# Kernel tuning notes

Hardware: AMD Instinct MI355X
Metric: run time of the kernel (lower is better)

## Reference

```python
import jax, jax.numpy as jnp
import numpy as np

B, S, D, H = 4, 8192, 1024, 16
DK = D // H
EPS = 1e-6


def setup_inputs() -> dict:
    key = jax.random.key(0)
    ks = jax.random.split(key, 9)
    s = 1.0 / np.sqrt(D)
    return {
        "x": jax.random.normal(ks[0], (B, S, D), dtype=jnp.float32),
        "Wq": jax.random.normal(ks[1], (D, D), dtype=jnp.float32) * s,
        "bq": jax.random.normal(ks[2], (D,), dtype=jnp.float32) * s,
        "Wk": jax.random.normal(ks[3], (D, D), dtype=jnp.float32) * s,
        "bk": jax.random.normal(ks[4], (D,), dtype=jnp.float32) * s,
        "Wv": jax.random.normal(ks[5], (D, D), dtype=jnp.float32) * s,
        "bv": jax.random.normal(ks[6], (D,), dtype=jnp.float32) * s,
        "Wo": jax.random.normal(ks[7], (D, D), dtype=jnp.float32) * s,
        "bo": jax.random.normal(ks[8], (D,), dtype=jnp.float32) * s,
    }


def reference(x, Wq, bq, Wk, bk, Wv, bv, Wo, bo):
    # projections (torch Linear: x @ W.T + b), split heads -> [B, H, S, DK]
    def proj(W, b):
        return (x @ W.T + b).reshape(B, S, H, DK).transpose(0, 2, 1, 3)

    q = jax.nn.relu(proj(Wq, bq)) + EPS
    k = jax.nn.relu(proj(Wk, bk)) + EPS
    v = proj(Wv, bv)

    # kv state: [B, H, DK, DK]
    kv = jnp.einsum('bhsd,bhse->bhde', k, v)
    qkv = jnp.einsum('bhsd,bhde->bhse', q, kv)            # [B, H, S, DK]
    k_sum = k.sum(axis=2)                                  # [B, H, DK]
    q_k_sum = jnp.einsum('bhsd,bhd->bhs', q, k_sum)        # [B, H, S]
    out = qkv / (q_k_sum[..., None] + EPS)                 # [B, H, S, DK]

    out = out.transpose(0, 2, 1, 3).reshape(B, S, D)
    return out @ Wo.T + bo
```

## Files before the change

### kernel.cpp

```cpp
#include <hip/hip_runtime.h>
#include <hip/hip_bf16.h>

#define BB 4
#define SS 8192
#define DD 1024
#define HH 16
#define DKK 64
#define EPSV 1e-6f

typedef unsigned short u16;
typedef __attribute__((ext_vector_type(8))) short bf16x8v;
typedef __attribute__((ext_vector_type(4))) float f32x4v;

__device__ inline u16 f2bf(float f) {
    __hip_bfloat16 b = __float2bfloat16(f);
    return *reinterpret_cast<u16*>(&b);
}
__device__ inline float bf2f(u16 u) {
    union { unsigned int i; float f; } c; c.i = ((unsigned int)u) << 16; return c.f;
}

__device__ inline void gload_lds16(const void* g, void* l) {
    __builtin_amdgcn_global_load_lds(
        (const __attribute__((address_space(1))) void*)g,
        (__attribute__((address_space(3))) void*)l, 16, 0, 0);
}

__global__ __launch_bounds__(256)
void split_hilo(const float* __restrict__ in, u16* __restrict__ outp, int n4) {
    int i = blockIdx.x * 256 + threadIdx.x;
    if (i >= n4) return;
    size_t e = (size_t)i * 4;
    size_t row = e >> 10; int col = (int)(e & 1023);
    float4 v = *(const float4*)&in[e];
    ushort4 hi, lo;
    hi.x = f2bf(v.x); lo.x = f2bf(v.x - bf2f(hi.x));
    hi.y = f2bf(v.y); lo.y = f2bf(v.y - bf2f(hi.y));
    hi.z = f2bf(v.z); lo.z = f2bf(v.z - bf2f(hi.z));
    hi.w = f2bf(v.w); lo.w = f2bf(v.w - bf2f(hi.w));
    size_t ob = row * 2048 + col;
    *(ushort4*)&outp[ob] = hi;
    *(ushort4*)&outp[ob + 1024] = lo;
}

template<int EPI>
__global__ __launch_bounds__(512, 2)
void gemm_split(const u16* __restrict__ A, const u16* __restrict__ Wsp,
                const float* __restrict__ bias, void* __restrict__ out) {
    __shared__ u16 lds[65536];

    int bid = blockIdx.x;
    int tl  = (bid & 7) * 64 + (bid >> 3);
    const int m0 = (tl >> 2) * 256;
    const int n0 = (tl & 3) * 256;

    const int tid = threadIdx.x;
    const int w = tid >> 6, l = tid & 63;
    const int wr = (w >> 2) * 128;
    const int wc = (w & 3) * 64;
    const int aReg = (w >> 2) * 8192;
    const int bReg = 16384 + ((w & 3) >> 1) * 8192;
    const int bLoc = ((w & 3) & 1) * 64;

    f32x4v acc[8][4];
    #pragma unroll
    for (int i = 0; i < 8; ++i)
        #pragma unroll
        for (int j = 0; j < 4; ++j) acc[i][j] = (f32x4v)0.f;

    const int srow = l >> 3;
    const int scol = ((l & 7) ^ srow) << 3;

    const u16* Abase = A   + (size_t)m0 * 2048;
    const u16* Bbase = Wsp + (size_t)n0 * 2048;

    auto kaOf = [](int t) { int k0 = t * 64; return (k0 < 2048) ? k0 : k0 - 2048; };
    auto kwOf = [](int t) { int k0 = t * 64; return (k0 < 1024) ? k0 : k0 - 1024; };

    auto stageA = [&](int t, int half) {
        if (t >= 48) return;
        const u16* src = Abase + (size_t)(half * 128) * 2048 + kaOf(t) + scol;
        u16* dst = &lds[(t & 1) * 32768 + half * 8192];
        #pragma unroll
        for (int g = 0; g < 2; ++g) {
            int chunk = g * 8 + w;
            gload_lds16(src + (size_t)(chunk * 8 + srow) * 2048, dst + chunk * 512);
        }
    };
    auto stageB = [&](int t, int half) {
        if (t >= 48) return;
        const u16* src = Bbase + (size_t)(half * 128) * 2048 + kwOf(t) + scol;
        u16* dst = &lds[(t & 1) * 32768 + 16384 + half * 8192];
        #pragma unroll
        for (int g = 0; g < 2; ++g) {
            int chunk = g * 8 + w;
            gload_lds16(src + (size_t)(chunk * 8 + srow) * 2048, dst + chunk * 512);
        }
    };

    stageA(0, 0); stageA(0, 1); stageB(0, 0); stageB(0, 1);
    stageB(1, 0); stageB(1, 1);
    asm volatile("s_waitcnt vmcnt(4)" ::: "memory");
    __builtin_amdgcn_s_barrier();

    for (int t = 0; t < 48; ++t) {
        __builtin_amdgcn_sched_barrier(0);
        const char* aRg = (const char*)&lds[(t & 1) * 32768 + aReg];
        const char* bRg = (const char*)&lds[(t & 1) * 32768 + bReg];
        const int cb = (l >> 4) << 4;

        bf16x8v bF[4][2], aF[2][2];
        #pragma unroll
        for (int fn = 0; fn < 4; ++fn)
            #pragma unroll
            for (int ks = 0; ks < 2; ++ks) {
                int r = bLoc + fn * 16 + (l & 15);
                bF[fn][ks] = *(const bf16x8v*)(bRg + r * 128 + ((ks * 64 + cb) ^ ((r & 7) << 4)));
            }
        #pragma unroll
        for (int f = 0; f < 2; ++f)
            #pragma unroll
            for (int ks = 0; ks < 2; ++ks) {
                int r = f * 16 + (l & 15);
                aF[f][ks] = *(const bf16x8v*)(aRg + r * 128 + ((ks * 64 + cb) ^ ((r & 7) << 4)));
            }
        stageA(t + 1, 0);
        __builtin_amdgcn_s_barrier();
        asm volatile("s_waitcnt lgkmcnt(0)" ::: "memory");
        __builtin_amdgcn_s_setprio(1);
        #pragma unroll
        for (int f = 0; f < 2; ++f)
            #pragma unroll
            for (int fn = 0; fn < 4; ++fn)
                #pragma unroll
                for (int ks = 0; ks < 2; ++ks)
                    acc[f][fn] = __builtin_amdgcn_mfma_f32_16x16x32_bf16(
                        aF[f][ks], bF[fn][ks], acc[f][fn], 0, 0, 0);
        __builtin_amdgcn_s_setprio(0);
        __builtin_amdgcn_s_barrier();

        #pragma unroll
        for (int q = 1; q < 4; ++q) {
            #pragma unroll
            for (int f = 0; f < 2; ++f)
                #pragma unroll
                for (int ks = 0; ks < 2; ++ks) {
                    int r = q * 32 + f * 16 + (l & 15);
                    aF[f][ks] = *(const bf16x8v*)(aRg + r * 128 + ((ks * 64 + cb) ^ ((r & 7) << 4)));
                }
            if (q == 1)      stageA(t + 1, 1);
            else if (q == 2) stageB(t + 2, 0);
            else             stageB(t + 2, 1);
            __builtin_amdgcn_s_barrier();
            asm volatile("s_waitcnt lgkmcnt(0)" ::: "memory");
            __builtin_amdgcn_s_setprio(1);
            #pragma unroll
            for (int f = 0; f < 2; ++f)
                #pragma unroll
                for (int fn = 0; fn < 4; ++fn)
                    #pragma unroll
                    for (int ks = 0; ks < 2; ++ks)
                        acc[q * 2 + f][fn] = __builtin_amdgcn_mfma_f32_16x16x32_bf16(
                            aF[f][ks], bF[fn][ks], acc[q * 2 + f][fn], 0, 0, 0);
            __builtin_amdgcn_s_setprio(0);
            if (q == 3) asm volatile("s_waitcnt vmcnt(4)" ::: "memory");
            __builtin_amdgcn_s_barrier();
        }
    }

    float bv4[4];
    #pragma unroll
    for (int fn = 0; fn < 4; ++fn) bv4[fn] = bias[n0 + wc + fn * 16 + (l & 15)];

    #pragma unroll
    for (int mf = 0; mf < 8; ++mf)
        #pragma unroll
        for (int fn = 0; fn < 4; ++fn)
            #pragma unroll
            for (int r = 0; r < 4; ++r) {
                int m = m0 + wr + mf * 16 + ((l >> 4) << 2) + r;
                int n = n0 + wc + fn * 16 + (l & 15);
                float o = acc[mf][fn][r] + bv4[fn];
                if (EPI == 0 || EPI == 1) o = fmaxf(o, 0.f) + EPSV;
                if (EPI <= 2) {
                    int b = m >> 13, s = m & (SS - 1), h = n >> 6, d = n & 63;
                    size_t idx = (((size_t)b * HH + h) * SS + s) * DKK + d;
                    if (EPI == 0) ((float*)out)[idx] = o;
                    else          ((u16*)out)[idx]   = f2bf(o);
                } else {
                    ((float*)out)[(size_t)m * DD + n] = o;
                }
            }
}

__global__ __launch_bounds__(256)
void kv_ksum_kernel(const u16* __restrict__ k, const u16* __restrict__ v,
                    float* __restrict__ kv, float* __restrict__ ksum) {
    __shared__ float kt[64][64];
    __shared__ float vt[64][64];
    const int bh = blockIdx.y;
    const int tid = threadIdx.x;
    const int d0 = (tid >> 4) << 2;
    const int e0 = (tid & 15) << 2;
    float acc[4][4];
    #pragma unroll
    for (int i = 0; i < 4; ++i)
        #pragma unroll
        for (int j = 0; j < 4; ++j) acc[i][j] = 0.f;
    float ksl = 0.f;

    const size_t base = ((size_t)bh * SS + (size_t)blockIdx.x * 512) * DKK;
    for (int sub = 0; sub < 8; ++sub) {
        #pragma unroll
        for (int it = 0; it < 4; ++it) {
            int f = tid + it * 256;
            int r = f >> 4, c = (f & 15) << 2;
            ushort4 ku = *(const ushort4*)&k[base + sub * 4096 + (size_t)r * 64 + c];
            ushort4 vu = *(const ushort4*)&v[base + sub * 4096 + (size_t)r * 64 + c];
            *(float4*)&kt[r][c] = make_float4(bf2f(ku.x), bf2f(ku.y), bf2f(ku.z), bf2f(ku.w));
            *(float4*)&vt[r][c] = make_float4(bf2f(vu.x), bf2f(vu.y), bf2f(vu.z), bf2f(vu.w));
        }
        __syncthreads();
        for (int ss = 0; ss < 64; ++ss) {
            float4 ka = *(const float4*)&kt[ss][d0];
            float4 va = *(const float4*)&vt[ss][e0];
            float ar[4] = {ka.x, ka.y, ka.z, ka.w};
            float vr[4] = {va.x, va.y, va.z, va.w};
            #pragma unroll
            for (int i = 0; i < 4; ++i)
                #pragma unroll
                for (int j = 0; j < 4; ++j)
                    acc[i][j] = fmaf(ar[i], vr[j], acc[i][j]);
        }
        if (tid < 64) {
            for (int ss = 0; ss < 64; ++ss) ksl += kt[ss][tid];
        }
        __syncthreads();
    }
    float* kvb = kv + (size_t)bh * 4096;
    #pragma unroll
    for (int i = 0; i < 4; ++i)
        #pragma unroll
        for (int j = 0; j < 4; ++j)
            atomicAdd(&kvb[(d0 + i) * 64 + (e0 + j)], acc[i][j]);
    if (tid < 64) atomicAdd(&ksum[bh * 64 + tid], ksl);
}

__global__ __launch_bounds__(256)
void qkv_norm_kernel(const float* __restrict__ q, const float* __restrict__ kv,
                     const float* __restrict__ ksum, u16* __restrict__ mid) {
    __shared__ float kvs[64][65];
    __shared__ float ks[64];
    __shared__ float qrow[4][64];
    const int bh = blockIdx.y, b = bh >> 4, h = bh & 15;
    const int tid = threadIdx.x;
    for (int i = tid; i < 4096; i += 256) kvs[i >> 6][i & 63] = kv[(size_t)bh * 4096 + i];
    if (tid < 64) ks[tid] = ksum[bh * 64 + tid];
    __syncthreads();
    const int g = tid >> 6, lane = tid & 63;
    float kvc[64];
    #pragma unroll
    for (int d = 0; d < 64; ++d) kvc[d] = kvs[d][lane];
    const float ksl = ks[lane];
    const size_t qbase = (size_t)bh * SS * DKK;
    const int s0 = blockIdx.x * 256;
    for (int it = 0; it < 64; ++it) {
        int s = s0 + (it << 2) + g;
        float qv = q[qbase + (size_t)s * DKK + lane];
        qrow[g][lane] = qv;
        float qks = qv * ksl;
        #pragma unroll
        for (int off = 32; off >= 1; off >>= 1) qks += __shfl_xor(qks, off, 64);
        float o = 0.f;
        #pragma unroll
        for (int d4 = 0; d4 < 64; d4 += 4) {
            float4 qq = *(const float4*)&qrow[g][d4];
            o = fmaf(qq.x, kvc[d4 + 0], o);
            o = fmaf(qq.y, kvc[d4 + 1], o);
            o = fmaf(qq.z, kvc[d4 + 2], o);
            o = fmaf(qq.w, kvc[d4 + 3], o);
        }
        o = o / (qks + EPSV);
        u16 hi = f2bf(o);
        u16 lo = f2bf(o - bf2f(hi));
        size_t ob = ((size_t)b * SS + s) * 2048 + h * DKK + lane;
        mid[ob] = hi;
        mid[ob + 1024] = lo;
    }
}

extern "C" void kernel_launch(void* const* d_in, const int* in_sizes, int n_in,
                              void* d_out, int out_size, void* d_ws, size_t ws_size,
                              hipStream_t stream) {
    const float* x  = (const float*)d_in[0];
    const float* Wq = (const float*)d_in[1];
    const float* bq = (const float*)d_in[2];
    const float* Wk = (const float*)d_in[3];
    const float* bk = (const float*)d_in[4];
    const float* Wv = (const float*)d_in[5];
    const float* bv = (const float*)d_in[6];
    const float* Wo = (const float*)d_in[7];
    const float* bo = (const float*)d_in[8];

    char* ws = (char*)d_ws;
    u16*   xsplit  = (u16*)ws;
    u16*   wsplit  = (u16*)(ws + 134217728);
    u16*   k_ws    = (u16*)(ws + 138412032);
    u16*   v_ws    = (u16*)(ws + 205520896);
    float* kv_ws   = (float*)(ws + 272629760);
    float* ksum_ws = (float*)(ws + 273678336);
    u16*   midsplit = xsplit;
    float* q_ws    = (float*)d_out;

    split_hilo<<<32768, 256, 0, stream>>>(x, xsplit, 8388608);

    split_hilo<<<1024, 256, 0, stream>>>(Wq, wsplit, 262144);
    gemm_split<0><<<512, 512, 0, stream>>>(xsplit, wsplit, bq, (void*)q_ws);
    split_hilo<<<1024, 256, 0, stream>>>(Wk, wsplit, 262144);
    gemm_split<1><<<512, 512, 0, stream>>>(xsplit, wsplit, bk, (void*)k_ws);
    split_hilo<<<1024, 256, 0, stream>>>(Wv, wsplit, 262144);
    gemm_split<2><<<512, 512, 0, stream>>>(xsplit, wsplit, bv, (void*)v_ws);

    hipMemsetAsync(kv_ws, 0, 1048576 + 16384, stream);
    kv_ksum_kernel<<<dim3(16, 64), 256, 0, stream>>>(k_ws, v_ws, kv_ws, ksum_ws);
    qkv_norm_kernel<<<dim3(32, 64), 256, 0, stream>>>(q_ws, kv_ws, ksum_ws, midsplit);

    split_hilo<<<1024, 256, 0, stream>>>(Wo, wsplit, 262144);
    gemm_split<3><<<512, 512, 0, stream>>>(midsplit, wsplit, bo, d_out);
}
```

Before: 1.180 ms.

## Fuse K/V projections, fold q·ksum into Q GEMM epilogue, rework kv reduction

The K and V projections become one GEMM over a concatenated 2048-wide weight. The Q projection now runs after the kv/ksum pass, so its epilogue can compute the per-row q·ksum normaliser and the norm kernel no longer needs a shuffle reduction. The GEMM inner loop is reordered to load 4 A fragments against 2 B fragments per phase, and the kv reduction kernel now uses async LDS staging with 8x8 per-thread tiles and an in-block reduction before the atomics. This is meant to cut launches, redundant A-matrix reads and atomic traffic, at the cost of more register pressure and a new workspace layout.

```diff
diff --git a/kernel.cpp b/kernel.cpp
--- a/kernel.cpp
+++ b/kernel.cpp
@@ -43,16 +43,19 @@
     *(ushort4*)&outp[ob + 1024] = lo;
 }
 
-template<int EPI>
+template<int EPI, int NT>
 __global__ __launch_bounds__(512, 2)
 void gemm_split(const u16* __restrict__ A, const u16* __restrict__ Wsp,
-                const float* __restrict__ bias, void* __restrict__ out) {
+                const float* __restrict__ bias, const float* __restrict__ bias2,
+                void* __restrict__ out, void* __restrict__ out2,
+                const float* __restrict__ ksum, float* __restrict__ qks) {
     __shared__ u16 lds[65536];
 
+    constexpr int CHUNK = 128 * NT / 8;
     int bid = blockIdx.x;
-    int tl  = (bid & 7) * 64 + (bid >> 3);
-    const int m0 = (tl >> 2) * 256;
-    const int n0 = (tl & 3) * 256;
+    int tl  = (bid & 7) * CHUNK + (bid >> 3);
+    const int m0 = (tl / NT) * 256;
+    const int n0 = (tl % NT) * 256;
 
     const int tid = threadIdx.x;
     const int w = tid >> 6, l = tid & 63;
@@ -104,173 +107,278 @@
     __builtin_amdgcn_s_barrier();
 
     for (int t = 0; t < 48; ++t) {
-        __builtin_amdgcn_sched_barrier(0);
         const char* aRg = (const char*)&lds[(t & 1) * 32768 + aReg];
         const char* bRg = (const char*)&lds[(t & 1) * 32768 + bReg];
         const int cb = (l >> 4) << 4;
 
-        bf16x8v bF[4][2], aF[2][2];
-        #pragma unroll
-        for (int fn = 0; fn < 4; ++fn)
-            #pragma unroll
-            for (int ks = 0; ks < 2; ++ks) {
-                int r = bLoc + fn * 16 + (l & 15);
-                bF[fn][ks] = *(const bf16x8v*)(bRg + r * 128 + ((ks * 64 + cb) ^ ((r & 7) << 4)));
-            }
-        #pragma unroll
-        for (int f = 0; f < 2; ++f)
+        bf16x8v aF[4][2], bF0[2][2], bF1[2][2];
+        #pragma unroll
+        for (int f = 0; f < 4; ++f)
             #pragma unroll
             for (int ks = 0; ks < 2; ++ks) {
                 int r = f * 16 + (l & 15);
                 aF[f][ks] = *(const bf16x8v*)(aRg + r * 128 + ((ks * 64 + cb) ^ ((r & 7) << 4)));
             }
+        #pragma unroll
+        for (int f = 0; f < 2; ++f)
+            #pragma unroll
+            for (int ks = 0; ks < 2; ++ks) {
+                int r = bLoc + f * 16 + (l & 15);
+                bF0[f][ks] = *(const bf16x8v*)(bRg + r * 128 + ((ks * 64 + cb) ^ ((r & 7) << 4)));
+            }
         stageA(t + 1, 0);
         __builtin_amdgcn_s_barrier();
         asm volatile("s_waitcnt lgkmcnt(0)" ::: "memory");
         __builtin_amdgcn_s_setprio(1);
         #pragma unroll
-        for (int f = 0; f < 2; ++f)
-            #pragma unroll
-            for (int fn = 0; fn < 4; ++fn)
+        for (int f = 0; f < 4; ++f)
+            #pragma unroll
+            for (int fn = 0; fn < 2; ++fn)
                 #pragma unroll
                 for (int ks = 0; ks < 2; ++ks)
                     acc[f][fn] = __builtin_amdgcn_mfma_f32_16x16x32_bf16(
-                        aF[f][ks], bF[fn][ks], acc[f][fn], 0, 0, 0);
+                        aF[f][ks], bF0[fn][ks], acc[f][fn], 0, 0, 0);
         __builtin_amdgcn_s_setprio(0);
         __builtin_amdgcn_s_barrier();
 
         #pragma unroll
-        for (int q = 1; q < 4; ++q) {
-            #pragma unroll
-            for (int f = 0; f < 2; ++f)
-                #pragma unroll
-                for (int ks = 0; ks < 2; ++ks) {
-                    int r = q * 32 + f * 16 + (l & 15);
-                    aF[f][ks] = *(const bf16x8v*)(aRg + r * 128 + ((ks * 64 + cb) ^ ((r & 7) << 4)));
+        for (int f = 0; f < 2; ++f)
+            #pragma unroll
+            for (int ks = 0; ks < 2; ++ks) {
+                int r = bLoc + (2 + f) * 16 + (l & 15);
+                bF1[f][ks] = *(const bf16x8v*)(bRg + r * 128 + ((ks * 64 + cb) ^ ((r & 7) << 4)));
+            }
+        stageA(t + 1, 1);
+        __builtin_amdgcn_s_barrier();
+        asm volatile("s_waitcnt lgkmcnt(0)" ::: "memory");
+        __builtin_amdgcn_s_setprio(1);
+        #pragma unroll
+        for (int f = 0; f < 4; ++f)
+            #pragma unroll
+            for (int fn = 0; fn < 2; ++fn)
+                #pragma unroll
+                for (int ks = 0; ks < 2; ++ks)
+                    acc[f][2 + fn] = __builtin_amdgcn_mfma_f32_16x16x32_bf16(
+                        aF[f][ks], bF1[fn][ks], acc[f][2 + fn], 0, 0, 0);
+        __builtin_amdgcn_s_setprio(0);
+        __builtin_amdgcn_s_barrier();
+
+        #pragma unroll
+        for (int f = 0; f < 4; ++f)
+            #pragma unroll
+            for (int ks = 0; ks < 2; ++ks) {
+                int r = (4 + f) * 16 + (l & 15);
+                aF[f][ks] = *(const bf16x8v*)(aRg + r * 128 + ((ks * 64 + cb) ^ ((r & 7) << 4)));
+            }
+        stageB(t + 2, 0);
+        __builtin_amdgcn_s_barrier();
+        asm volatile("s_waitcnt lgkmcnt(0)" ::: "memory");
+        __builtin_amdgcn_s_setprio(1);
+        #pragma unroll
+        for (int f = 0; f < 4; ++f)
+            #pragma unroll
+            for (int fn = 0; fn < 2; ++fn)
+                #pragma unroll
+                for (int ks = 0; ks < 2; ++ks)
+                    acc[4 + f][fn] = __builtin_amdgcn_mfma_f32_16x16x32_bf16(
+                        aF[f][ks], bF0[fn][ks], acc[4 + f][fn], 0, 0, 0);
+        __builtin_amdgcn_s_setprio(0);
+        __builtin_amdgcn_s_barrier();
+
+        stageB(t + 2, 1);
+        __builtin_amdgcn_s_barrier();
+        __builtin_amdgcn_s_setprio(1);
+        #pragma unroll
+        for (int f = 0; f < 4; ++f)
+            #pragma unroll
+            for (int fn = 0; fn < 2; ++fn)
+                #pragma unroll
+                for (int ks = 0; ks < 2; ++ks)
+                    acc[4 + f][2 + fn] = __builtin_amdgcn_mfma_f32_16x16x32_bf16(
+                        aF[f][ks], bF1[fn][ks], acc[4 + f][2 + fn], 0, 0, 0);
+        __builtin_amdgcn_s_setprio(0);
+        asm volatile("s_waitcnt vmcnt(4)" ::: "memory");
+        __builtin_amdgcn_s_barrier();
+    }
+
+    const int lane15 = l & 15, lg = l >> 4;
+
+    if (EPI == 1) {
+        const bool isK = (n0 + wc) < 1024;
+        const int nb = (n0 + wc) - (isK ? 0 : 1024);
+        const float* bp = isK ? bias : bias2;
+        u16* outp = (u16*)(isK ? out : out2);
+        const int h = nb >> 6;
+        float bv4[4];
+        #pragma unroll
+        for (int fn = 0; fn < 4; ++fn) bv4[fn] = bp[nb + fn * 16 + lane15];
+        #pragma unroll
+        for (int mf = 0; mf < 8; ++mf)
+            #pragma unroll
+            for (int fn = 0; fn < 4; ++fn)
+                #pragma unroll
+                for (int r = 0; r < 4; ++r) {
+                    int m = m0 + wr + mf * 16 + lg * 4 + r;
+                    int b = m >> 13, s = m & (SS - 1);
+                    float o = acc[mf][fn][r] + bv4[fn];
+                    if (isK) o = fmaxf(o, 0.f) + EPSV;
+                    outp[(((size_t)b * HH + h) * SS + s) * DKK + fn * 16 + lane15] = f2bf(o);
                 }
-            if (q == 1)      stageA(t + 1, 1);
-            else if (q == 2) stageB(t + 2, 0);
-            else             stageB(t + 2, 1);
-            __builtin_amdgcn_s_barrier();
-            asm volatile("s_waitcnt lgkmcnt(0)" ::: "memory");
-            __builtin_amdgcn_s_setprio(1);
-            #pragma unroll
-            for (int f = 0; f < 2; ++f)
-                #pragma unroll
-                for (int fn = 0; fn < 4; ++fn)
-                    #pragma unroll
-                    for (int ks = 0; ks < 2; ++ks)
-                        acc[q * 2 + f][fn] = __builtin_amdgcn_mfma_f32_16x16x32_bf16(
-                            aF[f][ks], bF[fn][ks], acc[q * 2 + f][fn], 0, 0, 0);
-            __builtin_amdgcn_s_setprio(0);
-            if (q == 3) asm volatile("s_waitcnt vmcnt(4)" ::: "memory");
-            __builtin_amdgcn_s_barrier();
-        }
-    }
-
-    float bv4[4];
-    #pragma unroll
-    for (int fn = 0; fn < 4; ++fn) bv4[fn] = bias[n0 + wc + fn * 16 + (l & 15)];
-
-    #pragma unroll
-    for (int mf = 0; mf < 8; ++mf)
-        #pragma unroll
-        for (int fn = 0; fn < 4; ++fn)
+    } else if (EPI == 0) {
+        const int b = m0 >> 13, h = (n0 + wc) >> 6;
+        const int bh = b * HH + h;
+        float bv4[4], ksc[4];
+        #pragma unroll
+        for (int fn = 0; fn < 4; ++fn) {
+            bv4[fn] = bias[n0 + wc + fn * 16 + lane15];
+            ksc[fn] = ksum[(size_t)bh * 64 + fn * 16 + lane15];
+        }
+        float* qo = (float*)out;
+        #pragma unroll
+        for (int mf = 0; mf < 8; ++mf)
             #pragma unroll
             for (int r = 0; r < 4; ++r) {
-                int m = m0 + wr + mf * 16 + ((l >> 4) << 2) + r;
-                int n = n0 + wc + fn * 16 + (l & 15);
-                float o = acc[mf][fn][r] + bv4[fn];
-                if (EPI == 0 || EPI == 1) o = fmaxf(o, 0.f) + EPSV;
-                if (EPI <= 2) {
-                    int b = m >> 13, s = m & (SS - 1), h = n >> 6, d = n & 63;
-                    size_t idx = (((size_t)b * HH + h) * SS + s) * DKK + d;
-                    if (EPI == 0) ((float*)out)[idx] = o;
-                    else          ((u16*)out)[idx]   = f2bf(o);
-                } else {
-                    ((float*)out)[(size_t)m * DD + n] = o;
+                int m = m0 + wr + mf * 16 + lg * 4 + r;
+                int s = m & (SS - 1);
+                float part = 0.f;
+                #pragma unroll
+                for (int fn = 0; fn < 4; ++fn) {
+                    float o = fmaxf(acc[mf][fn][r] + bv4[fn], 0.f) + EPSV;
+                    qo[((size_t)bh * SS + s) * DKK + fn * 16 + lane15] = o;
+                    part += o * ksc[fn];
                 }
-            }
+                #pragma unroll
+                for (int msk = 1; msk < 16; msk <<= 1)
+                    part += __shfl_xor(part, msk, 16);
+                if (lane15 == 0) qks[(size_t)bh * SS + s] = part;
+            }
+    } else {
+        float bv4[4];
+        #pragma unroll
+        for (int fn = 0; fn < 4; ++fn) bv4[fn] = bias[n0 + wc + fn * 16 + lane15];
+        float* op = (float*)out;
+        #pragma unroll
+        for (int mf = 0; mf < 8; ++mf)
+            #pragma unroll
+            for (int fn = 0; fn < 4; ++fn)
+                #pragma unroll
+                for (int r = 0; r < 4; ++r) {
+                    int m = m0 + wr + mf * 16 + lg * 4 + r;
+                    op[(size_t)m * DD + n0 + wc + fn * 16 + lane15] = acc[mf][fn][r] + bv4[fn];
+                }
+    }
 }
 
 __global__ __launch_bounds__(256)
-void kv_ksum_kernel(const u16* __restrict__ k, const u16* __restrict__ v,
-                    float* __restrict__ kv, float* __restrict__ ksum) {
-    __shared__ float kt[64][64];
-    __shared__ float vt[64][64];
+void kv_ksum2(const u16* __restrict__ k, const u16* __restrict__ v,
+              float* __restrict__ kv, float* __restrict__ ksum) {
+    __shared__ u16 kb[2][4096];
+    __shared__ u16 vb[2][4096];
+    __shared__ float red[8192];
     const int bh = blockIdx.y;
     const int tid = threadIdx.x;
-    const int d0 = (tid >> 4) << 2;
-    const int e0 = (tid & 15) << 2;
-    float acc[4][4];
+    const int w = tid >> 6, l = tid & 63;
+    const int d0 = (l >> 3) * 8, e0 = (l & 7) * 8;
+    const size_t base = ((size_t)bh * SS + (size_t)blockIdx.x * 1024) * DKK;
+
+    float acc[8][8];
     #pragma unroll
-    for (int i = 0; i < 4; ++i)
-        #pragma unroll
-        for (int j = 0; j < 4; ++j) acc[i][j] = 0.f;
-    float ksl = 0.f;
-
-    const size_t base = ((size_t)bh * SS + (size_t)blockIdx.x * 512) * DKK;
-    for (int sub = 0; sub < 8; ++sub) {
-        #pragma unroll
-        for (int it = 0; it < 4; ++it) {
-            int f = tid + it * 256;
-            int r = f >> 4, c = (f & 15) << 2;
-            ushort4 ku = *(const ushort4*)&k[base + sub * 4096 + (size_t)r * 64 + c];
-            ushort4 vu = *(const ushort4*)&v[base + sub * 4096 + (size_t)r * 64 + c];
-            *(float4*)&kt[r][c] = make_float4(bf2f(ku.x), bf2f(ku.y), bf2f(ku.z), bf2f(ku.w));
-            *(float4*)&vt[r][c] = make_float4(bf2f(vu.x), bf2f(vu.y), bf2f(vu.z), bf2f(vu.w));
-        }
+    for (int i = 0; i < 8; ++i)
+        #pragma unroll
+        for (int j = 0; j < 8; ++j) acc[i][j] = 0.f;
+    float ksl[8];
+    #pragma unroll
+    for (int i = 0; i < 8; ++i) ksl[i] = 0.f;
+
+    auto stage = [&](int j, int buf) {
+        const u16* ksrc = k + base + (size_t)j * 4096;
+        const u16* vsrc = v + base + (size_t)j * 4096;
+        #pragma unroll
+        for (int g = 0; g < 2; ++g) {
+            int c = g * 4 + w;
+            gload_lds16(ksrc + c * 512 + (size_t)l * 8, &kb[buf][c * 512]);
+            gload_lds16(vsrc + c * 512 + (size_t)l * 8, &vb[buf][c * 512]);
+        }
+    };
+
+    stage(0, 0);
+    asm volatile("s_waitcnt vmcnt(0)" ::: "memory");
+    __syncthreads();
+    for (int j = 0; j < 16; ++j) {
+        if (j < 15) stage(j + 1, (j + 1) & 1);
+        const int buf = j & 1;
+        #pragma unroll 4
+        for (int i = 0; i < 16; ++i) {
+            int ss = w * 16 + i;
+            bf16x8v ku = *(const bf16x8v*)&kb[buf][ss * 64 + d0];
+            bf16x8v vu = *(const bf16x8v*)&vb[buf][ss * 64 + e0];
+            float ar[8], vr[8];
+            #pragma unroll
+            for (int q = 0; q < 8; ++q) { ar[q] = bf2f((u16)ku[q]); vr[q] = bf2f((u16)vu[q]); }
+            #pragma unroll
+            for (int q = 0; q < 8; ++q) ksl[q] += ar[q];
+            #pragma unroll
+            for (int ii = 0; ii < 8; ++ii)
+                #pragma unroll
+                for (int jj = 0; jj < 8; ++jj)
+                    acc[ii][jj] = fmaf(ar[ii], vr[jj], acc[ii][jj]);
+        }
+        asm volatile("s_waitcnt vmcnt(0)" ::: "memory");
         __syncthreads();
-        for (int ss = 0; ss < 64; ++ss) {
-            float4 ka = *(const float4*)&kt[ss][d0];
-            float4 va = *(const float4*)&vt[ss][e0];
-            float ar[4] = {ka.x, ka.y, ka.z, ka.w};
-            float vr[4] = {va.x, va.y, va.z, va.w};
-            #pragma unroll
-            for (int i = 0; i < 4; ++i)
-                #pragma unroll
-                for (int j = 0; j < 4; ++j)
-                    acc[i][j] = fmaf(ar[i], vr[j], acc[i][j]);
-        }
-        if (tid < 64) {
-            for (int ss = 0; ss < 64; ++ss) ksl += kt[ss][tid];
-        }
+    }
+
+    #pragma unroll
+    for (int half = 0; half < 2; ++half) {
         __syncthreads();
-    }
-    float* kvb = kv + (size_t)bh * 4096;
-    #pragma unroll
-    for (int i = 0; i < 4; ++i)
-        #pragma unroll
-        for (int j = 0; j < 4; ++j)
-            atomicAdd(&kvb[(d0 + i) * 64 + (e0 + j)], acc[i][j]);
-    if (tid < 64) atomicAdd(&ksum[bh * 64 + tid], ksl);
+        if ((d0 >> 5) == half) {
+            #pragma unroll
+            for (int ii = 0; ii < 8; ++ii) {
+                #pragma unroll
+                for (int j4 = 0; j4 < 2; ++j4)
+                    *(float4*)&red[w * 2048 + ((d0 & 31) + ii) * 64 + e0 + j4 * 4] =
+                        *(float4*)&acc[ii][j4 * 4];
+            }
+        }
+        __syncthreads();
+        float* kvb = kv + (size_t)bh * 4096 + half * 2048;
+        #pragma unroll
+        for (int u = 0; u < 8; ++u) {
+            int o = u * 256 + tid;
+            float s4 = red[o] + red[2048 + o] + red[4096 + o] + red[6144 + o];
+            atomicAdd(&kvb[o], s4);
+        }
+    }
+    __syncthreads();
+    if (e0 == 0) {
+        #pragma unroll
+        for (int ii = 0; ii < 8; ++ii) red[w * 64 + d0 + ii] = ksl[ii];
+    }
+    __syncthreads();
+    if (tid < 64)
+        atomicAdd(&ksum[(size_t)bh * 64 + tid],
+                  red[tid] + red[64 + tid] + red[128 + tid] + red[192 + tid]);
 }
 
 __global__ __launch_bounds__(256)
-void qkv_norm_kernel(const float* __restrict__ q, const float* __restrict__ kv,
-                     const float* __restrict__ ksum, u16* __restrict__ mid) {
+void qkv_norm2(const float* __restrict__ q, const float* __restrict__ kvm,
+               const float* __restrict__ qks, u16* __restrict__ mid) {
     __shared__ float kvs[64][65];
-    __shared__ float ks[64];
     __shared__ float qrow[4][64];
     const int bh = blockIdx.y, b = bh >> 4, h = bh & 15;
     const int tid = threadIdx.x;
-    for (int i = tid; i < 4096; i += 256) kvs[i >> 6][i & 63] = kv[(size_t)bh * 4096 + i];
-    if (tid < 64) ks[tid] = ksum[bh * 64 + tid];
+    for (int i = tid; i < 4096; i += 256) kvs[i >> 6][i & 63] = kvm[(size_t)bh * 4096 + i];
     __syncthreads();
     const int g = tid >> 6, lane = tid & 63;
     float kvc[64];
     #pragma unroll
     for (int d = 0; d < 64; ++d) kvc[d] = kvs[d][lane];
-    const float ksl = ks[lane];
     const size_t qbase = (size_t)bh * SS * DKK;
     const int s0 = blockIdx.x * 256;
     for (int it = 0; it < 64; ++it) {
         int s = s0 + (it << 2) + g;
         float qv = q[qbase + (size_t)s * DKK + lane];
         qrow[g][lane] = qv;
-        float qks = qv * ksl;
-        #pragma unroll
-        for (int off = 32; off >= 1; off >>= 1) qks += __shfl_xor(qks, off, 64);
+        float den = qks[(size_t)bh * SS + s] + EPSV;
         float o = 0.f;
         #pragma unroll
         for (int d4 = 0; d4 < 64; d4 += 4) {
@@ -280,7 +388,7 @@
             o = fmaf(qq.z, kvc[d4 + 2], o);
             o = fmaf(qq.w, kvc[d4 + 3], o);
         }
-        o = o / (qks + EPSV);
+        o = o / den;
         u16 hi = f2bf(o);
         u16 lo = f2bf(o - bf2f(hi));
         size_t ob = ((size_t)b * SS + s) * 2048 + h * DKK + lane;
@@ -304,27 +412,30 @@
 
     char* ws = (char*)d_ws;
     u16*   xsplit  = (u16*)ws;
-    u16*   wsplit  = (u16*)(ws + 134217728);
-    u16*   k_ws    = (u16*)(ws + 138412032);
-    u16*   v_ws    = (u16*)(ws + 205520896);
-    float* kv_ws   = (float*)(ws + 272629760);
-    float* ksum_ws = (float*)(ws + 273678336);
+    u16*   wsp     = (u16*)(ws + 134217728);
+    float* qks_ws  = (float*)(ws + 134217728 + 4194304);
+    u16*   k_ws    = (u16*)(ws + 142606336);
+    u16*   v_ws    = (u16*)(ws + 209715200);
+    float* kv_ws   = (float*)(ws + 276824064);
+    float* ksum_ws = (float*)(ws + 277872640);
     u16*   midsplit = xsplit;
     float* q_ws    = (float*)d_out;
 
     split_hilo<<<32768, 256, 0, stream>>>(x, xsplit, 8388608);
-
-    split_hilo<<<1024, 256, 0, stream>>>(Wq, wsplit, 262144);
-    gemm_split<0><<<512, 512, 0, stream>>>(xsplit, wsplit, bq, (void*)q_ws);
-    split_hilo<<<1024, 256, 0, stream>>>(Wk, wsplit, 262144);
-    gemm_split<1><<<512, 512, 0, stream>>>(xsplit, wsplit, bk, (void*)k_ws);
-    split_hilo<<<1024, 256, 0, stream>>>(Wv, wsplit, 262144);
-    gemm_split<2><<<512, 512, 0, stream>>>(xsplit, wsplit, bv, (void*)v_ws);
-
+    split_hilo<<<1024, 256, 0, stream>>>(Wk, wsp, 262144);
+    split_hilo<<<1024, 256, 0, stream>>>(Wv, wsp + (size_t)1024 * 2048, 262144);
     hipMemsetAsync(kv_ws, 0, 1048576 + 16384, stream);
-    kv_ksum_kernel<<<dim3(16, 64), 256, 0, stream>>>(k_ws, v_ws, kv_ws, ksum_ws);
-    qkv_norm_kernel<<<dim3(32, 64), 256, 0, stream>>>(q_ws, kv_ws, ksum_ws, midsplit);
-
-    split_hilo<<<1024, 256, 0, stream>>>(Wo, wsplit, 262144);
-    gemm_split<3><<<512, 512, 0, stream>>>(midsplit, wsplit, bo, d_out);
-}
+
+    gemm_split<1, 8><<<1024, 512, 0, stream>>>(xsplit, wsp, bk, bv,
+                                               (void*)k_ws, (void*)v_ws, nullptr, nullptr);
+    kv_ksum2<<<dim3(8, 64), 256, 0, stream>>>(k_ws, v_ws, kv_ws, ksum_ws);
+
+    split_hilo<<<1024, 256, 0, stream>>>(Wq, wsp, 262144);
+    gemm_split<0, 4><<<512, 512, 0, stream>>>(xsplit, wsp, bq, nullptr,
+                                              (void*)q_ws, nullptr, ksum_ws, qks_ws);
+    qkv_norm2<<<dim3(32, 64), 256, 0, stream>>>(q_ws, kv_ws, qks_ws, midsplit);
+
+    split_hilo<<<1024, 256, 0, stream>>>(Wo, wsp, 262144);
+    gemm_split<3, 4><<<512, 512, 0, stream>>>(midsplit, wsp, bo, nullptr,
+                                              d_out, nullptr, nullptr, nullptr);
+}
```

Measured after the change: 1.152 ms. 2.4% less time.
